# Kernel optimization log

Hardware: AMD Instinct MI355X
Metric: run time of the kernel (lower is better)

Reference implementation:

```python
import jax, jax.numpy as jnp
import numpy as np

B, T, D, E, K = 4, 2048, 1024, 8, 2

def setup_inputs() -> dict:
    key = jax.random.key(0)
    ks = jax.random.split(key, 4)
    scale = 1.0 / np.sqrt(D)
    return {
        "input_feat": jax.random.normal(ks[0], (B, T, D), dtype=jnp.float32),
        "delta": jax.random.normal(ks[1], (B, T, D), dtype=jnp.float32),
        "gate_W": jax.random.normal(ks[2], (E, D), dtype=jnp.float32) * scale,
        "gate_b": jnp.zeros((E,), dtype=jnp.float32),
        "expert_W": jax.random.normal(ks[3], (E, D, D), dtype=jnp.float32) * scale,
        "expert_b": jnp.zeros((E, D), dtype=jnp.float32),
    }

def reference(input_feat, delta, gate_W, gate_b, expert_W, expert_b):
    # Gating: logits [B,T,E], top-k over experts, softmax over the k logits
    gate_logits = jnp.einsum("btd,ed->bte", input_feat, gate_W) + gate_b
    topk_vals, topk_idx = jax.lax.top_k(gate_logits, K)          # [B,T,K]
    topk_weights = jax.nn.softmax(topk_vals, axis=-1)            # [B,T,K]

    # Dense per-expert linear on delta: [B,T,D,E] (torch Linear: x @ W.T + b)
    expert_outputs = jnp.einsum("btd,efd->btfe", delta, expert_W) + expert_b.T

    # Gather top-k expert outputs and weighted-combine
    idx = jnp.broadcast_to(topk_idx[:, :, None, :], (B, T, D, K))
    topk_outputs = jnp.take_along_axis(expert_outputs, idx, axis=-1)  # [B,T,D,K]
    weighted_output = jnp.sum(topk_outputs * topk_weights[:, :, None, :], axis=-1)
    return weighted_output
```

## Files before the change

### kernel.cpp

```cpp
#include <hip/hip_runtime.h>
#include <stdint.h>

#define NTOK 8192
#define D 1024
#define E 8
#define BM 128
#define BN 128
#define BK 32

typedef __attribute__((ext_vector_type(8))) short short8;
typedef __attribute__((ext_vector_type(4))) float f32x4;

__device__ __forceinline__ ushort f2bf(float f) {
  uint32_t x = __float_as_uint(f);
  x += 0x7FFFu + ((x >> 16) & 1u);
  return (ushort)(x >> 16);
}

__global__ __launch_bounds__(256) void convert_bf16_kernel(
    const float* __restrict__ src, ushort* __restrict__ dst, int n4) {
  int i = blockIdx.x * 256 + threadIdx.x;
  if (i >= n4) return;
  float4 v = ((const float4*)src)[i];
  ushort4 u;
  u.x = f2bf(v.x); u.y = f2bf(v.y); u.z = f2bf(v.z); u.w = f2bf(v.w);
  ((ushort4*)dst)[i] = u;
}

__global__ __launch_bounds__(256) void gate_topk_kernel(
    const float* __restrict__ x,
    const float* __restrict__ gW,
    const float* __restrict__ gb,
    int*   __restrict__ idx01,
    float2* __restrict__ w01)
{
  int wave = threadIdx.x >> 6;
  int lane = threadIdx.x & 63;
  int t = blockIdx.x * 4 + wave;

  const float4* xr = (const float4*)(x + (size_t)t * D) + lane * 4;
  float acc[E];
#pragma unroll
  for (int e = 0; e < E; ++e) acc[e] = 0.f;
#pragma unroll
  for (int q = 0; q < 4; ++q) {
    float4 xv = xr[q];
#pragma unroll
    for (int e = 0; e < E; ++e) {
      float4 wv = ((const float4*)(gW + e * D))[lane * 4 + q];
      acc[e] += xv.x * wv.x + xv.y * wv.y + xv.z * wv.z + xv.w * wv.w;
    }
  }
#pragma unroll
  for (int e = 0; e < E; ++e) {
    float v = acc[e];
#pragma unroll
    for (int off = 32; off > 0; off >>= 1) v += __shfl_xor(v, off, 64);
    acc[e] = v;
  }
  if (lane == 0) {
    float lg[E];
#pragma unroll
    for (int e = 0; e < E; ++e) lg[e] = acc[e] + gb[e];
    int i0 = 0; float v0 = lg[0];
#pragma unroll
    for (int e = 1; e < E; ++e) { if (lg[e] > v0) { v0 = lg[e]; i0 = e; } }
    int i1 = -1; float v1 = -1e30f;
#pragma unroll
    for (int e = 0; e < E; ++e) { if (e != i0 && lg[e] > v1) { v1 = lg[e]; i1 = e; } }
    float e1 = __expf(v1 - v0);
    float inv = 1.f / (1.f + e1);
    idx01[t] = i0 | (i1 << 16);
    w01[t] = make_float2(inv, e1 * inv);
  }
}

__global__ __launch_bounds__(256) void bin_kernel(
    const int*    __restrict__ idx01,
    const float2* __restrict__ w01,
    int*   __restrict__ cnt,
    int*   __restrict__ list,
    float* __restrict__ wlist)
{
  __shared__ int hist[E];
  __shared__ int base[E];
  int tid = threadIdx.x;
  int t = blockIdx.x * 256 + tid;
  if (tid < E) hist[tid] = 0;
  __syncthreads();

  int packed = idx01[t];
  float2 w = w01[t];
  int i0 = packed & 0xFFFF, i1 = packed >> 16;
  int r0 = atomicAdd(&hist[i0], 1);
  int r1 = atomicAdd(&hist[i1], 1);
  __syncthreads();
  if (tid < E) base[tid] = atomicAdd(&cnt[tid], hist[tid]);
  __syncthreads();

  int s0 = base[i0] + r0;
  list[i0 * NTOK + s0] = t; wlist[i0 * NTOK + s0] = w.x;
  int s1 = base[i1] + r1;
  list[i1 * NTOK + s1] = t; wlist[i1 * NTOK + s1] = w.y;
}

__global__ __launch_bounds__(256) void moe_gemm_kernel(
    const ushort* __restrict__ Db,
    const ushort* __restrict__ Wb,
    const float*  __restrict__ eb,
    const int*    __restrict__ cnt,
    const int*    __restrict__ list,
    const float*  __restrict__ wlist,
    float*        __restrict__ out)
{
  const int MT = NTOK / BM;
  const int NTI = D / BN;
  int bx = blockIdx.x;
  int e = bx / (MT * NTI);
  int rem = bx - e * (MT * NTI);
  int mt = rem / NTI;
  int nt = rem - mt * NTI;
  int M = cnt[e];
  int m0 = mt * BM;
  if (m0 >= M) return;
  int n0 = nt * BN;

  __shared__ ushort As[BM * BK];
  __shared__ ushort Bs[BN * BK];

  int tid = threadIdx.x;
  int wave = tid >> 6;
  int lane = tid & 63;
  int wm = wave >> 1;
  int wn = wave & 1;
  const int c = lane & 15;
  const int q = lane >> 4;

  const int* listE = list + e * NTOK;

  const ushort* aptr[2];
  ushort* alds[2];
#pragma unroll
  for (int p = 0; p < 2; ++p) {
    int r = m0 + p * 64 + wave * 16 + (lane >> 2);
    int tok = listE[r < M ? r : m0];
    aptr[p] = Db + (size_t)tok * D + ((lane & 3) << 3);
    alds[p] = &As[(p * 64 + wave * 16) * BK];
  }

  const ushort* WbE = Wb + ((size_t)e << 20);
  const ushort* bptr[2];
  ushort* blds[2];
#pragma unroll
  for (int sub = 0; sub < 2; ++sub) {
    int row = wave * 32 + sub * 16 + (lane >> 2);
    bptr[sub] = WbE + (size_t)(n0 + row) * D + ((lane & 3) << 3);
    blds[sub] = &Bs[(wave * 32 + sub * 16) * BK];
  }

  f32x4 acc[4][4];
#pragma unroll
  for (int i = 0; i < 4; ++i)
#pragma unroll
    for (int j = 0; j < 4; ++j)
      acc[i][j] = (f32x4){0.f, 0.f, 0.f, 0.f};

  for (int k0 = 0; k0 < D; k0 += BK) {
#pragma unroll
    for (int p = 0; p < 2; ++p) {
      __builtin_amdgcn_global_load_lds(
          (const __attribute__((address_space(1))) void*)(aptr[p] + k0),
          (__attribute__((address_space(3))) void*)alds[p], 16, 0, 0);
    }
#pragma unroll
    for (int sub = 0; sub < 2; ++sub) {
      __builtin_amdgcn_global_load_lds(
          (const __attribute__((address_space(1))) void*)(bptr[sub] + k0),
          (__attribute__((address_space(3))) void*)blds[sub], 16, 0, 0);
    }
    __syncthreads();

    short8 a[4], b[4];
#pragma unroll
    for (int i = 0; i < 4; ++i) {
      a[i] = *(const short8*)&As[(wm * 64 + i * 16 + c) * BK + q * 8];
      b[i] = *(const short8*)&Bs[(wn * 64 + i * 16 + c) * BK + q * 8];
    }
#pragma unroll
    for (int i = 0; i < 4; ++i)
#pragma unroll
      for (int j = 0; j < 4; ++j)
        acc[i][j] = __builtin_amdgcn_mfma_f32_16x16x32_bf16(a[i], b[j], acc[i][j], 0, 0, 0);
    __syncthreads();
  }

  float bias[4];
#pragma unroll
  for (int j = 0; j < 4; ++j)
    bias[j] = eb[e * D + n0 + wn * 64 + j * 16 + c];
  const float* wlE = wlist + e * NTOK;
#pragma unroll
  for (int i = 0; i < 4; ++i) {
#pragma unroll
    for (int r = 0; r < 4; ++r) {
      int m = m0 + wm * 64 + i * 16 + q * 4 + r;
      if (m < M) {
        int tok = listE[m];
        float w = wlE[m];
        float* orow = out + (size_t)tok * D + n0 + wn * 64 + c;
#pragma unroll
        for (int j = 0; j < 4; ++j)
          atomicAdd(&orow[j * 16], (acc[i][j][r] + bias[j]) * w);
      }
    }
  }
}

extern "C" void kernel_launch(void* const* d_in, const int* in_sizes, int n_in,
                              void* d_out, int out_size, void* d_ws, size_t ws_size,
                              hipStream_t stream) {
  const float* input_feat = (const float*)d_in[0];
  const float* delta      = (const float*)d_in[1];
  const float* gate_W     = (const float*)d_in[2];
  const float* gate_b     = (const float*)d_in[3];
  const float* expert_W   = (const float*)d_in[4];
  const float* expert_b   = (const float*)d_in[5];
  float* out = (float*)d_out;

  char* ws = (char*)d_ws;
  ushort* Wb    = (ushort*)ws;
  ushort* Db    = (ushort*)(ws + 16777216);
  char*   meta  = ws + 2 * 16777216;
  int*    cnt   = (int*)meta;
  int*    list  = (int*)(meta + 256);
  float*  wlist = (float*)(meta + 256 + NTOK * E * 4);
  int*    idx01 = (int*)(meta + 256 + 2 * NTOK * E * 4);
  float2* w01   = (float2*)(meta + 256 + 2 * NTOK * E * 4 + NTOK * 4);

  hipMemsetAsync(d_out, 0, (size_t)NTOK * D * sizeof(float), stream);
  hipMemsetAsync(cnt, 0, E * sizeof(int), stream);

  int nW4 = E * D * D / 4;
  int nD4 = NTOK * D / 4;
  convert_bf16_kernel<<<(nW4 + 255) / 256, 256, 0, stream>>>(expert_W, Wb, nW4);
  convert_bf16_kernel<<<(nD4 + 255) / 256, 256, 0, stream>>>(delta, Db, nD4);
  gate_topk_kernel<<<NTOK / 4, 256, 0, stream>>>(input_feat, gate_W, gate_b, idx01, w01);
  bin_kernel<<<NTOK / 256, 256, 0, stream>>>(idx01, w01, cnt, list, wlist);
  moe_gemm_kernel<<<E * (NTOK / BM) * (D / BN), 256, 0, stream>>>(
      Db, Wb, expert_b, cnt, list, wlist, out);
}
```

Baseline: 264.9 us.

## Retile MoE GEMM to 128x64x64 with XOR-swizzled LDS and fuse prep kernels

```diff
diff --git a/kernel.cpp b/kernel.cpp
--- a/kernel.cpp
+++ b/kernel.cpp
@@ -5,8 +5,8 @@
 #define D 1024
 #define E 8
 #define BM 128
-#define BN 128
-#define BK 32
+#define BN 64
+#define BK 64
 
 typedef __attribute__((ext_vector_type(8))) short short8;
 typedef __attribute__((ext_vector_type(4))) float f32x4;
@@ -17,23 +17,34 @@
   return (ushort)(x >> 16);
 }
 
-__global__ __launch_bounds__(256) void convert_bf16_kernel(
-    const float* __restrict__ src, ushort* __restrict__ dst, int n4) {
+#define NW4 2097152
+#define ND4 2097152
+#define NO4 2097152
+__global__ __launch_bounds__(256) void convert_zero_kernel(
+    const float* __restrict__ expert_W, const float* __restrict__ delta,
+    ushort* __restrict__ Wb, ushort* __restrict__ Db,
+    float* __restrict__ out, int* __restrict__ cnt) {
   int i = blockIdx.x * 256 + threadIdx.x;
-  if (i >= n4) return;
-  float4 v = ((const float4*)src)[i];
-  ushort4 u;
-  u.x = f2bf(v.x); u.y = f2bf(v.y); u.z = f2bf(v.z); u.w = f2bf(v.w);
-  ((ushort4*)dst)[i] = u;
+  if (i < E) cnt[i] = 0;
+  if (i < NW4) {
+    float4 v = ((const float4*)expert_W)[i];
+    ushort4 u; u.x = f2bf(v.x); u.y = f2bf(v.y); u.z = f2bf(v.z); u.w = f2bf(v.w);
+    ((ushort4*)Wb)[i] = u;
+  } else if (i < NW4 + ND4) {
+    int j = i - NW4;
+    float4 v = ((const float4*)delta)[j];
+    ushort4 u; u.x = f2bf(v.x); u.y = f2bf(v.y); u.z = f2bf(v.z); u.w = f2bf(v.w);
+    ((ushort4*)Db)[j] = u;
+  } else {
+    int j = i - NW4 - ND4;
+    ((float4*)out)[j] = (float4){0.f, 0.f, 0.f, 0.f};
+  }
 }
 
 __global__ __launch_bounds__(256) void gate_topk_kernel(
-    const float* __restrict__ x,
-    const float* __restrict__ gW,
+    const float* __restrict__ x, const float* __restrict__ gW,
     const float* __restrict__ gb,
-    int*   __restrict__ idx01,
-    float2* __restrict__ w01)
-{
+    int* __restrict__ idx01, float2* __restrict__ w01) {
   int wave = threadIdx.x >> 6;
   int lane = threadIdx.x & 63;
   int t = blockIdx.x * 4 + wave;
@@ -76,12 +87,8 @@
 }
 
 __global__ __launch_bounds__(256) void bin_kernel(
-    const int*    __restrict__ idx01,
-    const float2* __restrict__ w01,
-    int*   __restrict__ cnt,
-    int*   __restrict__ list,
-    float* __restrict__ wlist)
-{
+    const int* __restrict__ idx01, const float2* __restrict__ w01,
+    int* __restrict__ cnt, int* __restrict__ list, float* __restrict__ wlist) {
   __shared__ int hist[E];
   __shared__ int base[E];
   int tid = threadIdx.x;
@@ -105,21 +112,15 @@
 }
 
 __global__ __launch_bounds__(256) void moe_gemm_kernel(
-    const ushort* __restrict__ Db,
-    const ushort* __restrict__ Wb,
-    const float*  __restrict__ eb,
-    const int*    __restrict__ cnt,
-    const int*    __restrict__ list,
-    const float*  __restrict__ wlist,
-    float*        __restrict__ out)
-{
-  const int MT = NTOK / BM;
-  const int NTI = D / BN;
+    const ushort* __restrict__ Db, const ushort* __restrict__ Wb,
+    const float* __restrict__ eb, const int* __restrict__ cnt,
+    const int* __restrict__ list, const float* __restrict__ wlist,
+    float* __restrict__ out) {
   int bx = blockIdx.x;
-  int e = bx / (MT * NTI);
-  int rem = bx - e * (MT * NTI);
-  int mt = rem / NTI;
-  int nt = rem - mt * NTI;
+  int mt = bx >> 7;
+  int rem = bx & 127;
+  int e = rem >> 4;
+  int nt = rem & 15;
   int M = cnt[e];
   int m0 = mt * BM;
   if (m0 >= M) return;
@@ -138,66 +139,70 @@
 
   const int* listE = list + e * NTOK;
 
-  const ushort* aptr[2];
-  ushort* alds[2];
-#pragma unroll
-  for (int p = 0; p < 2; ++p) {
-    int r = m0 + p * 64 + wave * 16 + (lane >> 2);
+  int rloc = lane >> 3;
+  int gglob = (lane & 7) ^ rloc;
+  const ushort* aptr[4];
+  ushort* alds[4];
+#pragma unroll
+  for (int p = 0; p < 4; ++p) {
+    int r = m0 + wave * 32 + p * 8 + rloc;
     int tok = listE[r < M ? r : m0];
-    aptr[p] = Db + (size_t)tok * D + ((lane & 3) << 3);
-    alds[p] = &As[(p * 64 + wave * 16) * BK];
-  }
-
+    aptr[p] = Db + (size_t)tok * D + gglob * 8;
+    alds[p] = &As[(wave * 32 + p * 8) * BK];
+  }
   const ushort* WbE = Wb + ((size_t)e << 20);
   const ushort* bptr[2];
   ushort* blds[2];
 #pragma unroll
   for (int sub = 0; sub < 2; ++sub) {
-    int row = wave * 32 + sub * 16 + (lane >> 2);
-    bptr[sub] = WbE + (size_t)(n0 + row) * D + ((lane & 3) << 3);
-    blds[sub] = &Bs[(wave * 32 + sub * 16) * BK];
-  }
-
-  f32x4 acc[4][4];
+    int row = n0 + wave * 16 + sub * 8 + rloc;
+    bptr[sub] = WbE + (size_t)row * D + gglob * 8;
+    blds[sub] = &Bs[(wave * 16 + sub * 8) * BK];
+  }
+
+  f32x4 acc[4][2];
 #pragma unroll
   for (int i = 0; i < 4; ++i)
 #pragma unroll
-    for (int j = 0; j < 4; ++j)
+    for (int j = 0; j < 2; ++j)
       acc[i][j] = (f32x4){0.f, 0.f, 0.f, 0.f};
 
   for (int k0 = 0; k0 < D; k0 += BK) {
 #pragma unroll
-    for (int p = 0; p < 2; ++p) {
+    for (int p = 0; p < 4; ++p)
       __builtin_amdgcn_global_load_lds(
           (const __attribute__((address_space(1))) void*)(aptr[p] + k0),
           (__attribute__((address_space(3))) void*)alds[p], 16, 0, 0);
-    }
-#pragma unroll
-    for (int sub = 0; sub < 2; ++sub) {
+#pragma unroll
+    for (int sub = 0; sub < 2; ++sub)
       __builtin_amdgcn_global_load_lds(
           (const __attribute__((address_space(1))) void*)(bptr[sub] + k0),
           (__attribute__((address_space(3))) void*)blds[sub], 16, 0, 0);
+    __syncthreads();
+
+#pragma unroll
+    for (int s = 0; s < 2; ++s) {
+      int sw = (((s * 4 + q) ^ (c & 7)) * 8);
+      short8 a[4], b[2];
+#pragma unroll
+      for (int i = 0; i < 4; ++i)
+        a[i] = *(const short8*)&As[(wm * 64 + i * 16 + c) * BK + sw];
+#pragma unroll
+      for (int j = 0; j < 2; ++j)
+        b[j] = *(const short8*)&Bs[(wn * 32 + j * 16 + c) * BK + sw];
+#pragma unroll
+      for (int i = 0; i < 4; ++i)
+#pragma unroll
+        for (int j = 0; j < 2; ++j)
+          acc[i][j] = __builtin_amdgcn_mfma_f32_16x16x32_bf16(a[i], b[j], acc[i][j], 0, 0, 0);
     }
     __syncthreads();
-
-    short8 a[4], b[4];
-#pragma unroll
-    for (int i = 0; i < 4; ++i) {
-      a[i] = *(const short8*)&As[(wm * 64 + i * 16 + c) * BK + q * 8];
-      b[i] = *(const short8*)&Bs[(wn * 64 + i * 16 + c) * BK + q * 8];
-    }
-#pragma unroll
-    for (int i = 0; i < 4; ++i)
-#pragma unroll
-      for (int j = 0; j < 4; ++j)
-        acc[i][j] = __builtin_amdgcn_mfma_f32_16x16x32_bf16(a[i], b[j], acc[i][j], 0, 0, 0);
-    __syncthreads();
-  }
-
-  float bias[4];
-#pragma unroll
-  for (int j = 0; j < 4; ++j)
-    bias[j] = eb[e * D + n0 + wn * 64 + j * 16 + c];
+  }
+
+  float bias[2];
+#pragma unroll
+  for (int j = 0; j < 2; ++j)
+    bias[j] = eb[e * D + n0 + wn * 32 + j * 16 + c];
   const float* wlE = wlist + e * NTOK;
 #pragma unroll
   for (int i = 0; i < 4; ++i) {
@@ -207,9 +212,9 @@
       if (m < M) {
         int tok = listE[m];
         float w = wlE[m];
-        float* orow = out + (size_t)tok * D + n0 + wn * 64 + c;
-#pragma unroll
-        for (int j = 0; j < 4; ++j)
+        float* orow = out + (size_t)tok * D + n0 + wn * 32 + c;
+#pragma unroll
+        for (int j = 0; j < 2; ++j)
           atomicAdd(&orow[j * 16], (acc[i][j][r] + bias[j]) * w);
       }
     }
@@ -237,15 +242,10 @@
   int*    idx01 = (int*)(meta + 256 + 2 * NTOK * E * 4);
   float2* w01   = (float2*)(meta + 256 + 2 * NTOK * E * 4 + NTOK * 4);
 
-  hipMemsetAsync(d_out, 0, (size_t)NTOK * D * sizeof(float), stream);
-  hipMemsetAsync(cnt, 0, E * sizeof(int), stream);
-
-  int nW4 = E * D * D / 4;
-  int nD4 = NTOK * D / 4;
-  convert_bf16_kernel<<<(nW4 + 255) / 256, 256, 0, stream>>>(expert_W, Wb, nW4);
-  convert_bf16_kernel<<<(nD4 + 255) / 256, 256, 0, stream>>>(delta, Db, nD4);
+  int total4 = NW4 + ND4 + NO4;
+  convert_zero_kernel<<<total4 / 256, 256, 0, stream>>>(expert_W, delta, Wb, Db, out, cnt);
   gate_topk_kernel<<<NTOK / 4, 256, 0, stream>>>(input_feat, gate_W, gate_b, idx01, w01);
   bin_kernel<<<NTOK / 256, 256, 0, stream>>>(idx01, w01, cnt, list, wlist);
-  moe_gemm_kernel<<<E * (NTOK / BM) * (D / BN), 256, 0, stream>>>(
+  moe_gemm_kernel<<<(NTOK / BM) * 128, 256, 0, stream>>>(
       Db, Wb, expert_b, cnt, list, wlist, out);
 }
```

Result: faster. 236.8 us (-10.6%).
